# Kernel tuning notes

Hardware: AMD Instinct MI355X
Metric: run time of the kernel (lower is better)

Reference implementation:

```python
import jax, jax.numpy as jnp
import numpy as np

D = 4096
B_BITS = 4
NUM_CENTROIDS = 2 ** B_BITS  # 16 uniform centroids in [-1, 1]
N_TOKENS = 8192


def setup_inputs() -> dict:
    key = jax.random.key(0)
    kx, kp = jax.random.split(key)
    x = jax.random.normal(kx, (N_TOKENS, D), dtype=jnp.float32)
    # Orthogonal rotation Pi via QR of a random Gaussian (matches torch.linalg.qr)
    rand_mat = jax.random.normal(kp, (D, D), dtype=jnp.float32)
    Pi, _ = jnp.linalg.qr(rand_mat)
    centroids = jnp.linspace(-1.0, 1.0, NUM_CENTROIDS, dtype=jnp.float32)
    return {"x": x, "Pi": Pi, "centroids": centroids}


def _quantize(y, centroids):
    # Centroids are uniformly spaced on [-1, 1]; nearest-centroid argmin has the
    # closed form below (identical result to the broadcast |y - c| argmin, without
    # materializing the O(N*d*2^b) distance tensor).
    n = centroids.shape[0]
    scale = (n - 1) * 0.5
    idx = jnp.clip(jnp.round((y + 1.0) * scale), 0, n - 1).astype(jnp.int32)
    return centroids[idx]


def reference(x, Pi, centroids):
    y = x @ Pi.T                      # [N, d] rotate into quantization basis
    y_q = _quantize(y, centroids)     # nearest uniform centroid
    x_tilde = y_q @ Pi                # rotate back
    return x_tilde
```

## Files before the change

kernel.cpp:

```cpp
#include <hip/hip_runtime.h>
#include <hip/hip_bf16.h>

#define DD 4096
#define NTOK 8192

using u16 = unsigned short;

typedef __attribute__((ext_vector_type(8))) short bfrag;
typedef __attribute__((ext_vector_type(4))) float ffrag;
typedef __attribute__((ext_vector_type(4))) float f32x4v;

__device__ __forceinline__ u16 f2bf(float f) {
  unsigned u = __float_as_uint(f);
  u += 0x7FFFu + ((u >> 16) & 1u);
  return (u16)(u >> 16);
}
__device__ __forceinline__ float bf2f(u16 u) {
  return __uint_as_float(((unsigned)u) << 16);
}

#define GLDS16(g, l)                                                  \
  __builtin_amdgcn_global_load_lds(                                   \
      (__attribute__((address_space(1))) const void*)(g),             \
      (__attribute__((address_space(3))) void*)(l), 16, 0, 0)

#define MEMFENCE() asm volatile("" ::: "memory")

__global__ void __launch_bounds__(256) split_bf16_kernel(
    const float* __restrict__ in, u16* __restrict__ hi,
    u16* __restrict__ lo, long n4) {
  long i = (long)blockIdx.x * blockDim.x + threadIdx.x;
  const long stride = (long)gridDim.x * blockDim.x;
  for (; i < n4; i += stride) {
    f32x4v v = reinterpret_cast<const f32x4v*>(in)[i];
    u16 h[4], l[4];
#pragma unroll
    for (int j = 0; j < 4; ++j) {
      float f = v[j];
      u16 hb = f2bf(f);
      h[j] = hb;
      l[j] = f2bf(f - bf2f(hb));
    }
    ushort4 hv, lv;
    hv.x = h[0]; hv.y = h[1]; hv.z = h[2]; hv.w = h[3];
    lv.x = l[0]; lv.y = l[1]; lv.z = l[2]; lv.w = l[3];
    reinterpret_cast<ushort4*>(hi)[i] = hv;
    reinterpret_cast<ushort4*>(lo)[i] = lv;
  }
}

__global__ void __launch_bounds__(256) transpose_bf16_kernel(
    const float* __restrict__ in, u16* __restrict__ out, int R, int C) {
  __shared__ u16 tile[64][65];
  const int bc = blockIdx.x << 6;
  const int br = blockIdx.y << 6;
  const int tc = threadIdx.x & 63;
  const int tr0 = threadIdx.x >> 6;
#pragma unroll
  for (int p = 0; p < 16; ++p) {
    int r = tr0 + (p << 2);
    tile[tc][r] = f2bf(in[(size_t)(br + r) * C + (bc + tc)]);
  }
  __syncthreads();
#pragma unroll
  for (int p = 0; p < 16; ++p) {
    int orow = tr0 + (p << 2);
    out[(size_t)(bc + orow) * R + (br + tc)] = tile[orow][tc];
  }
}

__global__ void __launch_bounds__(512, 2) gemm_fused3_kernel(
    const u16* __restrict__ Ah_, const u16* __restrict__ Al_,
    const u16* __restrict__ Bh_, const u16* __restrict__ Bl_,
    u16* __restrict__ Yq, const float* __restrict__ cent, int M, int N) {
  __shared__ __align__(16) char SM[131072];
  __shared__ float clut[16];
  const int tid = threadIdx.x;
  if (tid < 16) clut[tid] = cent[tid];

  const int nbn = N >> 8;
  const int nwg = (M >> 8) * nbn;
  int wg = blockIdx.x;
  wg = (wg & 7) * (nwg >> 3) + (wg >> 3);
  const int tm = (wg / nbn) << 8;
  const int tn = (wg % nbn) << 8;

  const int lane = tid & 63;
  const int wv = tid >> 6;
  const int wm = wv >> 2;
  const int wn = wv & 3;
  const int l15 = lane & 15;
  const int kslc = lane >> 4;

  const int Dst = tid * 16;
  const int Lg = Dst ^ (((Dst >> 7) & 7) << 4);
  const int srow = Lg >> 6;
  const int scol = (Lg & 63) >> 1;
  const size_t sOffA = (size_t)(tm + srow) * 4096 + scol;
  const size_t sOffB = (size_t)(tn + srow) * 4096 + scol;

  auto STAGE = [&](int u, const u16* base, int tau) {
    if (tau >= 128) return;
    const u16* src = base + (u < 2 ? sOffA : sOffB) + tau * 32;
    char* lds = SM + (tau & 1) * 65536 + u * 16384 + Dst;
    GLDS16(src, lds);
    GLDS16(src + (size_t)128 * 4096, lds + 8192);
  };

  const int slot16 = ((((l15 & 1) << 2) | kslc) ^ (l15 >> 1)) << 4;
  const int aOff = wm * 8192 + (l15 >> 1) * 128 + slot16;
  const int bOff = wn * 4096 + (l15 >> 1) * 128 + slot16;

#define LDSF(b, ubase, off, f)                                           \
  (*reinterpret_cast<const bfrag*>(SM + (b) * 65536 + (ubase) + (off) +  \
                                   (f) * 1024))

  ffrag acc[8][4];
#pragma unroll
  for (int m = 0; m < 8; ++m)
#pragma unroll
    for (int n = 0; n < 4; ++n) acc[m][n] = {0.f, 0.f, 0.f, 0.f};

  bfrag Ahf[8], Alf[4], Bhf[4], Blf[4];

  STAGE(0, Ah_, 0); STAGE(1, Al_, 0); STAGE(2, Bh_, 0); STAGE(3, Bl_, 0);
  asm volatile("s_waitcnt vmcnt(2)" ::: "memory");
  MEMFENCE();
  __builtin_amdgcn_s_barrier();

#define MFMA16(Aset, a0, Bset, mb)                                       \
  __builtin_amdgcn_s_setprio(1);                                         \
  _Pragma("unroll")                                                      \
  for (int m = 0; m < 4; ++m)                                            \
    _Pragma("unroll")                                                    \
    for (int n = 0; n < 4; ++n)                                          \
      acc[(mb) + m][n] = __builtin_amdgcn_mfma_f32_16x16x32_bf16(        \
          Aset[(a0) + m], Bset[n], acc[(mb) + m][n], 0, 0, 0);           \
  __builtin_amdgcn_s_setprio(0);

  for (int t = 0; t < 128; ++t) {
    const int b = t & 1;
#pragma unroll
    for (int f = 0; f < 4; ++f) Ahf[f] = LDSF(b, 0, aOff, f);
#pragma unroll
    for (int f = 0; f < 4; ++f) Bhf[f] = LDSF(b, 32768, bOff, f);
    STAGE(0, Ah_, t + 1); STAGE(1, Al_, t + 1);
    MEMFENCE();
    __builtin_amdgcn_s_barrier();
    MFMA16(Ahf, 0, Bhf, 0)
    MEMFENCE();
    __builtin_amdgcn_s_barrier();
#pragma unroll
    for (int f = 0; f < 4; ++f) Ahf[4 + f] = LDSF(b, 0, aOff, 4 + f);
    STAGE(2, Bh_, t + 1); STAGE(3, Bl_, t + 1);
    MEMFENCE();
    __builtin_amdgcn_s_barrier();
    MFMA16(Ahf, 4, Bhf, 4)
    MEMFENCE();
    __builtin_amdgcn_s_barrier();
#pragma unroll
    for (int f = 0; f < 4; ++f) Alf[f] = LDSF(b, 16384, aOff, f);
    MEMFENCE();
    __builtin_amdgcn_s_barrier();
    MFMA16(Alf, 0, Bhf, 0)
    MEMFENCE();
    __builtin_amdgcn_s_barrier();
#pragma unroll
    for (int f = 0; f < 4; ++f) Alf[f] = LDSF(b, 16384, aOff, 4 + f);
    MEMFENCE();
    __builtin_amdgcn_s_barrier();
    MFMA16(Alf, 0, Bhf, 4)
    if (t < 127)
      asm volatile("s_waitcnt vmcnt(8)" ::: "memory");
    else
      asm volatile("s_waitcnt vmcnt(0)" ::: "memory");
    MEMFENCE();
    __builtin_amdgcn_s_barrier();
#pragma unroll
    for (int f = 0; f < 4; ++f) Blf[f] = LDSF(b, 49152, bOff, f);
    MEMFENCE();
    __builtin_amdgcn_s_barrier();
    MFMA16(Ahf, 0, Blf, 0)
    MFMA16(Ahf, 4, Blf, 4)
    asm volatile("s_waitcnt vmcnt(2)" ::: "memory");
    MEMFENCE();
    __builtin_amdgcn_s_barrier();
  }

  const int r0 = tm + wm * 128 + kslc * 4;
  const int c0 = tn + wn * 64 + l15;
#pragma unroll
  for (int m = 0; m < 8; ++m)
#pragma unroll
    for (int n = 0; n < 4; ++n)
#pragma unroll
      for (int r = 0; r < 4; ++r) {
        float y = acc[m][n][r];
        float s = rintf((y + 1.0f) * 7.5f);
        int idx = (int)s;
        idx = idx < 0 ? 0 : (idx > 15 ? 15 : idx);
        Yq[(size_t)(r0 + m * 16 + r) * N + (c0 + n * 16)] = f2bf(clut[idx]);
      }
#undef LDSF
#undef MFMA16
}

__global__ void __launch_bounds__(512, 2) gemm256_bt_kernel(
    const u16* __restrict__ A0, const u16* __restrict__ B0,
    float* __restrict__ Cout, int M, int N) {
  constexpr int NT = 64;
  __shared__ __align__(16) char SM[131072];
  const int tid = threadIdx.x;

  const int nbn = N >> 8;
  const int nwg = (M >> 8) * nbn;
  int wg = blockIdx.x;
  wg = (wg & 7) * (nwg >> 3) + (wg >> 3);
  const int tm = (wg / nbn) << 8;
  const int tn = (wg % nbn) << 8;

  const int lane = tid & 63;
  const int wv = tid >> 6;
  const int wm = wv >> 2;
  const int wn = wv & 3;
  const int l15 = lane & 15;
  const int kslc = lane >> 4;
  const int cXor = (lane & 7) << 4;

  const size_t thrOff =
      (size_t)(wv * 8 + (lane >> 3)) * 4096 + 8 * ((lane & 7) ^ (lane >> 3));
  const int ldsThr = wv * 1024 + lane * 16;

  auto STAGE = [&](int kind, int tau) {
    if (tau >= NT) return;
    const int b = tau & 1;
    const size_t ktE = (size_t)tau * 64;
    const u16* src;
    char* lds;
    if (kind >= 2) {
      const int idx = kind - 2;
      src = B0 + (size_t)(tn + idx * 128) * 4096 + ktE + thrOff;
      lds = SM + b * 65536 + 32768 + idx * 16384 + ldsThr;
    } else {
      src = A0 + (size_t)(tm + kind * 128) * 4096 + ktE + thrOff;
      lds = SM + b * 65536 + kind * 16384 + ldsThr;
    }
    GLDS16(src, lds);
    GLDS16(src + 262144, lds + 8192);
  };

#define LDSA(b, f, s)                                                      \
  (*reinterpret_cast<const bfrag*>(                                        \
      SM + (b) * 65536 + wm * 16384 + (((f) * 16 + l15) << 7) +            \
      ((((s) << 6) | (kslc << 4)) ^ cXor)))
#define LDSB(b, f, s)                                                      \
  (*reinterpret_cast<const bfrag*>(                                        \
      SM + (b) * 65536 + 32768 + (wn >> 1) * 16384 +                       \
      ((((wn & 1) * 64) + (f) * 16 + l15) << 7) +                          \
      ((((s) << 6) | (kslc << 4)) ^ cXor)))

  ffrag acc[8][4];
#pragma unroll
  for (int m = 0; m < 8; ++m)
#pragma unroll
    for (int n = 0; n < 4; ++n) acc[m][n] = {0.f, 0.f, 0.f, 0.f};

  STAGE(0, 0); STAGE(1, 0); STAGE(2, 0); STAGE(3, 0);
  STAGE(2, 1); STAGE(3, 1);
  asm volatile("s_waitcnt vmcnt(4)" ::: "memory");
  MEMFENCE();
  __builtin_amdgcn_s_barrier();

  bfrag Af[4], Bf[4];

  for (int t = 0; t < NT; ++t) {
    const int b = t & 1;
#pragma unroll
    for (int p = 0; p < 4; ++p) {
      const int s = p >> 1;
      const int mb = (p & 1) * 4;
      if ((p & 1) == 0) {
#pragma unroll
        for (int n = 0; n < 4; ++n) Bf[n] = LDSB(b, n, s);
      }
#pragma unroll
      for (int m = 0; m < 4; ++m) Af[m] = LDSA(b, mb + m, s);
      if (p == 0) STAGE(0, t + 1);
      else if (p == 1) STAGE(1, t + 1);
      else if (p == 3) { STAGE(2, t + 2); STAGE(3, t + 2); }
      MEMFENCE();
      __builtin_amdgcn_s_barrier();
      asm volatile("s_waitcnt lgkmcnt(0)" ::: "memory");
      __builtin_amdgcn_s_setprio(1);
#pragma unroll
      for (int m = 0; m < 4; ++m)
#pragma unroll
        for (int n = 0; n < 4; ++n)
          acc[mb + m][n] = __builtin_amdgcn_mfma_f32_16x16x32_bf16(
              Af[m], Bf[n], acc[mb + m][n], 0, 0, 0);
      __builtin_amdgcn_s_setprio(0);
      if (p == 3) {
        if (t == NT - 2)
          asm volatile("s_waitcnt vmcnt(0)" ::: "memory");
        else if (t < NT - 2)
          asm volatile("s_waitcnt vmcnt(4)" ::: "memory");
      }
      MEMFENCE();
      __builtin_amdgcn_s_barrier();
    }
  }

  const int r0 = tm + wm * 128 + kslc * 4;
  const int c0 = tn + wn * 64 + l15;
#pragma unroll
  for (int m = 0; m < 8; ++m)
#pragma unroll
    for (int n = 0; n < 4; ++n)
#pragma unroll
      for (int r = 0; r < 4; ++r)
        Cout[(size_t)(r0 + m * 16 + r) * N + (c0 + n * 16)] = acc[m][n][r];
#undef LDSA
#undef LDSB
}

extern "C" void kernel_launch(void* const* d_in, const int* in_sizes, int n_in,
                              void* d_out, int out_size, void* d_ws, size_t ws_size,
                              hipStream_t stream) {
  const float* x = (const float*)d_in[0];
  const float* Pi = (const float*)d_in[1];
  const float* cent = (const float*)d_in[2];
  float* out = (float*)d_out;

  const size_t MB = (size_t)1 << 20;
  if (ws_size < 288 * MB) return;

  char* ws = (char*)d_ws;
  u16* x_hi = (u16*)(ws + 0 * MB);
  u16* x_lo = (u16*)(ws + 64 * MB);
  u16* p_hi = (u16*)(ws + 128 * MB);
  u16* p_lo = (u16*)(ws + 160 * MB);
  u16* piT  = (u16*)(ws + 192 * MB);
  u16* yq   = (u16*)(ws + 224 * MB);

  split_bf16_kernel<<<2048, 256, 0, stream>>>(x, x_hi, x_lo, (long)NTOK * DD / 4);
  split_bf16_kernel<<<1024, 256, 0, stream>>>(Pi, p_hi, p_lo, (long)DD * DD / 4);
  transpose_bf16_kernel<<<dim3(DD / 64, DD / 64), 256, 0, stream>>>(Pi, piT, DD, DD);

  gemm_fused3_kernel<<<512, 512, 0, stream>>>(
      x_hi, x_lo, p_hi, p_lo, yq, cent, NTOK, DD);
  gemm256_bt_kernel<<<512, 512, 0, stream>>>(yq, piT, out, NTOK, DD);
}
```

Baseline: 1.014 ms.

## Replace bf16 low-part correction GEMMs with a single int8 MFMA correction term

The first GEMM used to compute three bf16 MFMA products (hi*hi, lo*hi, hi*lo) to emulate fp32 precision. It now computes hi*hi in bf16 and folds the two cross-correction terms into one int8 MFMA pass, using fixed-scale int8 quantizations of the x residual, x, Pi, and the Pi residual packed along K. Tiles shrink to 256x128 with a 1024-block grid and a reworked double-buffered staging schedule. The aim is to cut MFMA work and operand bandwidth for the correction terms. The cost is accuracy that depends on fixed quantization scales, which could misplace values near quantization boundaries.

```diff
diff --git a/kernel.cpp b/kernel.cpp
--- a/kernel.cpp
+++ b/kernel.cpp
@@ -7,6 +7,7 @@
 using u16 = unsigned short;
 
 typedef __attribute__((ext_vector_type(8))) short bfrag;
+typedef __attribute__((ext_vector_type(4))) int i32x4;
 typedef __attribute__((ext_vector_type(4))) float ffrag;
 typedef __attribute__((ext_vector_type(4))) float f32x4v;
 
@@ -18,6 +19,11 @@
 __device__ __forceinline__ float bf2f(u16 u) {
   return __uint_as_float(((unsigned)u) << 16);
 }
+__device__ __forceinline__ char q8(float v, float s) {
+  float r = rintf(v * s);
+  r = fminf(fmaxf(r, -127.f), 127.f);
+  return (char)(int)r;
+}
 
 #define GLDS16(g, l)                                                  \
   __builtin_amdgcn_global_load_lds(                                   \
@@ -26,26 +32,49 @@
 
 #define MEMFENCE() asm volatile("" ::: "memory")
 
-__global__ void __launch_bounds__(256) split_bf16_kernel(
+__global__ void __launch_bounds__(256) prep_x_kernel(
     const float* __restrict__ in, u16* __restrict__ hi,
-    u16* __restrict__ lo, long n4) {
+    char* __restrict__ lo8, char* __restrict__ hi8, long n4) {
   long i = (long)blockIdx.x * blockDim.x + threadIdx.x;
   const long stride = (long)gridDim.x * blockDim.x;
   for (; i < n4; i += stride) {
     f32x4v v = reinterpret_cast<const f32x4v*>(in)[i];
-    u16 h[4], l[4];
+    ushort4 hv; char4 lv, xv;
 #pragma unroll
     for (int j = 0; j < 4; ++j) {
       float f = v[j];
       u16 hb = f2bf(f);
-      h[j] = hb;
-      l[j] = f2bf(f - bf2f(hb));
-    }
-    ushort4 hv, lv;
-    hv.x = h[0]; hv.y = h[1]; hv.z = h[2]; hv.w = h[3];
-    lv.x = l[0]; lv.y = l[1]; lv.z = l[2]; lv.w = l[3];
+      float xl = f - bf2f(hb);
+      ((u16*)&hv)[j] = hb;
+      ((char*)&lv)[j] = q8(xl, 8192.f);
+      ((char*)&xv)[j] = q8(f, 16.f);
+    }
     reinterpret_cast<ushort4*>(hi)[i] = hv;
-    reinterpret_cast<ushort4*>(lo)[i] = lv;
+    reinterpret_cast<char4*>(lo8)[i] = lv;
+    reinterpret_cast<char4*>(hi8)[i] = xv;
+  }
+}
+
+__global__ void __launch_bounds__(256) prep_pi_kernel(
+    const float* __restrict__ in, u16* __restrict__ hi,
+    char* __restrict__ hi8, char* __restrict__ lo8, long n4) {
+  long i = (long)blockIdx.x * blockDim.x + threadIdx.x;
+  const long stride = (long)gridDim.x * blockDim.x;
+  for (; i < n4; i += stride) {
+    f32x4v v = reinterpret_cast<const f32x4v*>(in)[i];
+    ushort4 hv; char4 hq, lq;
+#pragma unroll
+    for (int j = 0; j < 4; ++j) {
+      float f = v[j];
+      u16 hb = f2bf(f);
+      float pl = f - bf2f(hb);
+      ((u16*)&hv)[j] = hb;
+      ((char*)&hq)[j] = q8(f, 1024.f);
+      ((char*)&lq)[j] = q8(pl, 524288.f);
+    }
+    reinterpret_cast<ushort4*>(hi)[i] = hv;
+    reinterpret_cast<char4*>(hi8)[i] = hq;
+    reinterpret_cast<char4*>(lo8)[i] = lq;
   }
 }
 
@@ -69,140 +98,150 @@
   }
 }
 
-__global__ void __launch_bounds__(512, 2) gemm_fused3_kernel(
-    const u16* __restrict__ Ah_, const u16* __restrict__ Al_,
-    const u16* __restrict__ Bh_, const u16* __restrict__ Bl_,
+__global__ void __launch_bounds__(512, 2) gemm_i8lo_kernel(
+    const u16* __restrict__ xh, const char* __restrict__ xl8,
+    const char* __restrict__ xh8, const u16* __restrict__ ph,
+    const char* __restrict__ ph8, const char* __restrict__ pl8,
     u16* __restrict__ Yq, const float* __restrict__ cent, int M, int N) {
-  __shared__ __align__(16) char SM[131072];
+  __shared__ __align__(16) char SM[98304];
   __shared__ float clut[16];
   const int tid = threadIdx.x;
   if (tid < 16) clut[tid] = cent[tid];
 
-  const int nbn = N >> 8;
+  const int nbn = N >> 7;
   const int nwg = (M >> 8) * nbn;
   int wg = blockIdx.x;
   wg = (wg & 7) * (nwg >> 3) + (wg >> 3);
   const int tm = (wg / nbn) << 8;
-  const int tn = (wg % nbn) << 8;
+  const int tn = (wg % nbn) << 7;
 
   const int lane = tid & 63;
   const int wv = tid >> 6;
-  const int wm = wv >> 2;
-  const int wn = wv & 3;
+  const int wm = wv >> 1;
+  const int wn = wv & 1;
   const int l15 = lane & 15;
   const int kslc = lane >> 4;
 
-  const int Dst = tid * 16;
-  const int Lg = Dst ^ (((Dst >> 7) & 7) << 4);
-  const int srow = Lg >> 6;
-  const int scol = (Lg & 63) >> 1;
-  const size_t sOffA = (size_t)(tm + srow) * 4096 + scol;
-  const size_t sOffB = (size_t)(tn + srow) * 4096 + scol;
-
-  auto STAGE = [&](int u, const u16* base, int tau) {
+  const int D0 = tid * 16, D1 = D0 + 8192;
+  const int L0 = D0 ^ (((D0 >> 7) & 3) << 4);
+  const int L1 = D1 ^ (((D1 >> 7) & 3) << 4);
+  const int row0 = D0 >> 6, row1 = D1 >> 6;
+  const int colE0 = (L0 & 63) >> 1, colE1 = (L1 & 63) >> 1;
+  const int sel0 = (L0 & 63) >> 5, col80 = L0 & 31;
+  const int sel1 = (L1 & 63) >> 5, col81 = L1 & 31;
+
+  const u16* pAh0 = xh + (size_t)(tm + row0) * 4096 + colE0;
+  const u16* pAh1 = xh + (size_t)(tm + row1) * 4096 + colE1;
+  const char* pA80 = (sel0 ? xh8 : xl8) + (size_t)(tm + row0) * 4096 + col80;
+  const char* pA81 = (sel1 ? xh8 : xl8) + (size_t)(tm + row1) * 4096 + col81;
+  const u16* pBh = ph + (size_t)(tn + row0) * 4096 + colE0;
+  const char* pB8 = (sel0 ? pl8 : ph8) + (size_t)(tn + row0) * 4096 + col80;
+
+  auto stageA = [&](int tau) {
     if (tau >= 128) return;
-    const u16* src = base + (u < 2 ? sOffA : sOffB) + tau * 32;
-    char* lds = SM + (tau & 1) * 65536 + u * 16384 + Dst;
-    GLDS16(src, lds);
-    GLDS16(src + (size_t)128 * 4096, lds + 8192);
+    char* base = SM + (tau & 1) * 49152;
+    const int o = tau * 32;
+    GLDS16(pAh0 + o, base + D0);
+    GLDS16(pAh1 + o, base + D0 + 8192);
+    GLDS16(pA80 + o, base + 16384 + D0);
+    GLDS16(pA81 + o, base + 16384 + D0 + 8192);
   };
-
-  const int slot16 = ((((l15 & 1) << 2) | kslc) ^ (l15 >> 1)) << 4;
-  const int aOff = wm * 8192 + (l15 >> 1) * 128 + slot16;
-  const int bOff = wn * 4096 + (l15 >> 1) * 128 + slot16;
-
-#define LDSF(b, ubase, off, f)                                           \
-  (*reinterpret_cast<const bfrag*>(SM + (b) * 65536 + (ubase) + (off) +  \
-                                   (f) * 1024))
-
-  ffrag acc[8][4];
-#pragma unroll
-  for (int m = 0; m < 8; ++m)
-#pragma unroll
-    for (int n = 0; n < 4; ++n) acc[m][n] = {0.f, 0.f, 0.f, 0.f};
-
-  bfrag Ahf[8], Alf[4], Bhf[4], Blf[4];
-
-  STAGE(0, Ah_, 0); STAGE(1, Al_, 0); STAGE(2, Bh_, 0); STAGE(3, Bl_, 0);
+  auto stageB = [&](int tau) {
+    if (tau >= 128) return;
+    char* base = SM + (tau & 1) * 49152;
+    const int o = tau * 32;
+    GLDS16(pBh + o, base + 32768 + D0);
+    GLDS16(pB8 + o, base + 40960 + D0);
+  };
+
+  int aoff[4], boff[4];
+#pragma unroll
+  for (int i = 0; i < 4; ++i) {
+    const int rA = wm * 64 + i * 16 + l15;
+    aoff[i] = rA * 64 + ((kslc ^ ((rA >> 1) & 3)) << 4);
+    const int rB = wn * 64 + i * 16 + l15;
+    boff[i] = rB * 64 + ((kslc ^ ((rB >> 1) & 3)) << 4);
+  }
+
+  ffrag acc[4][4];
+  i32x4 accq[4][4];
+#pragma unroll
+  for (int m = 0; m < 4; ++m)
+#pragma unroll
+    for (int n = 0; n < 4; ++n) {
+      acc[m][n] = {0.f, 0.f, 0.f, 0.f};
+      accq[m][n] = {0, 0, 0, 0};
+    }
+
+  stageA(0); stageB(0); stageB(1);
   asm volatile("s_waitcnt vmcnt(2)" ::: "memory");
   MEMFENCE();
   __builtin_amdgcn_s_barrier();
 
-#define MFMA16(Aset, a0, Bset, mb)                                       \
-  __builtin_amdgcn_s_setprio(1);                                         \
-  _Pragma("unroll")                                                      \
-  for (int m = 0; m < 4; ++m)                                            \
-    _Pragma("unroll")                                                    \
-    for (int n = 0; n < 4; ++n)                                          \
-      acc[(mb) + m][n] = __builtin_amdgcn_mfma_f32_16x16x32_bf16(        \
-          Aset[(a0) + m], Bset[n], acc[(mb) + m][n], 0, 0, 0);           \
-  __builtin_amdgcn_s_setprio(0);
+  bfrag Ahf[4], Bhf[4];
+  i32x4 A8f[4], B8f[4];
 
   for (int t = 0; t < 128; ++t) {
-    const int b = t & 1;
-#pragma unroll
-    for (int f = 0; f < 4; ++f) Ahf[f] = LDSF(b, 0, aOff, f);
-#pragma unroll
-    for (int f = 0; f < 4; ++f) Bhf[f] = LDSF(b, 32768, bOff, f);
-    STAGE(0, Ah_, t + 1); STAGE(1, Al_, t + 1);
+    const char* base = SM + (t & 1) * 49152;
+#pragma unroll
+    for (int i = 0; i < 4; ++i)
+      Ahf[i] = *reinterpret_cast<const bfrag*>(base + aoff[i]);
+#pragma unroll
+    for (int i = 0; i < 4; ++i)
+      Bhf[i] = *reinterpret_cast<const bfrag*>(base + 32768 + boff[i]);
+#pragma unroll
+    for (int i = 0; i < 4; ++i)
+      A8f[i] = *reinterpret_cast<const i32x4*>(base + 16384 + aoff[i]);
+#pragma unroll
+    for (int i = 0; i < 4; ++i)
+      B8f[i] = *reinterpret_cast<const i32x4*>(base + 40960 + boff[i]);
+    stageA(t + 1);
     MEMFENCE();
     __builtin_amdgcn_s_barrier();
-    MFMA16(Ahf, 0, Bhf, 0)
+    __builtin_amdgcn_s_setprio(1);
+#pragma unroll
+    for (int m = 0; m < 4; ++m)
+#pragma unroll
+      for (int n = 0; n < 4; ++n)
+        acc[m][n] = __builtin_amdgcn_mfma_f32_16x16x32_bf16(
+            Ahf[m], Bhf[n], acc[m][n], 0, 0, 0);
+    __builtin_amdgcn_s_setprio(0);
+    asm volatile("s_waitcnt lgkmcnt(0)" ::: "memory");
     MEMFENCE();
     __builtin_amdgcn_s_barrier();
-#pragma unroll
-    for (int f = 0; f < 4; ++f) Ahf[4 + f] = LDSF(b, 0, aOff, 4 + f);
-    STAGE(2, Bh_, t + 1); STAGE(3, Bl_, t + 1);
+    stageB(t + 2);
     MEMFENCE();
     __builtin_amdgcn_s_barrier();
-    MFMA16(Ahf, 4, Bhf, 4)
+    __builtin_amdgcn_s_setprio(1);
+#pragma unroll
+    for (int m = 0; m < 4; ++m)
+#pragma unroll
+      for (int n = 0; n < 4; ++n)
+        accq[m][n] = __builtin_amdgcn_mfma_i32_16x16x64_i8(
+            A8f[m], B8f[n], accq[m][n], 0, 0, 0);
+    __builtin_amdgcn_s_setprio(0);
+    if (t >= 126)
+      asm volatile("s_waitcnt vmcnt(0)" ::: "memory");
+    else
+      asm volatile("s_waitcnt vmcnt(2)" ::: "memory");
     MEMFENCE();
     __builtin_amdgcn_s_barrier();
-#pragma unroll
-    for (int f = 0; f < 4; ++f) Alf[f] = LDSF(b, 16384, aOff, f);
-    MEMFENCE();
-    __builtin_amdgcn_s_barrier();
-    MFMA16(Alf, 0, Bhf, 0)
-    MEMFENCE();
-    __builtin_amdgcn_s_barrier();
-#pragma unroll
-    for (int f = 0; f < 4; ++f) Alf[f] = LDSF(b, 16384, aOff, 4 + f);
-    MEMFENCE();
-    __builtin_amdgcn_s_barrier();
-    MFMA16(Alf, 0, Bhf, 4)
-    if (t < 127)
-      asm volatile("s_waitcnt vmcnt(8)" ::: "memory");
-    else
-      asm volatile("s_waitcnt vmcnt(0)" ::: "memory");
-    MEMFENCE();
-    __builtin_amdgcn_s_barrier();
-#pragma unroll
-    for (int f = 0; f < 4; ++f) Blf[f] = LDSF(b, 49152, bOff, f);
-    MEMFENCE();
-    __builtin_amdgcn_s_barrier();
-    MFMA16(Ahf, 0, Blf, 0)
-    MFMA16(Ahf, 4, Blf, 4)
-    asm volatile("s_waitcnt vmcnt(2)" ::: "memory");
-    MEMFENCE();
-    __builtin_amdgcn_s_barrier();
-  }
-
-  const int r0 = tm + wm * 128 + kslc * 4;
+  }
+
+  const int r0 = tm + wm * 64 + kslc * 4;
   const int c0 = tn + wn * 64 + l15;
 #pragma unroll
-  for (int m = 0; m < 8; ++m)
+  for (int m = 0; m < 4; ++m)
 #pragma unroll
     for (int n = 0; n < 4; ++n)
 #pragma unroll
       for (int r = 0; r < 4; ++r) {
-        float y = acc[m][n][r];
+        float y = acc[m][n][r] + (float)accq[m][n][r] * 0x1p-23f;
         float s = rintf((y + 1.0f) * 7.5f);
         int idx = (int)s;
         idx = idx < 0 ? 0 : (idx > 15 ? 15 : idx);
         Yq[(size_t)(r0 + m * 16 + r) * N + (c0 + n * 16)] = f2bf(clut[idx]);
       }
-#undef LDSF
-#undef MFMA16
 }
 
 __global__ void __launch_bounds__(512, 2) gemm256_bt_kernel(
@@ -335,18 +374,22 @@
   if (ws_size < 288 * MB) return;
 
   char* ws = (char*)d_ws;
-  u16* x_hi = (u16*)(ws + 0 * MB);
-  u16* x_lo = (u16*)(ws + 64 * MB);
-  u16* p_hi = (u16*)(ws + 128 * MB);
-  u16* p_lo = (u16*)(ws + 160 * MB);
-  u16* piT  = (u16*)(ws + 192 * MB);
-  u16* yq   = (u16*)(ws + 224 * MB);
-
-  split_bf16_kernel<<<2048, 256, 0, stream>>>(x, x_hi, x_lo, (long)NTOK * DD / 4);
-  split_bf16_kernel<<<1024, 256, 0, stream>>>(Pi, p_hi, p_lo, (long)DD * DD / 4);
+  u16* x_hi  = (u16*)(ws + 0 * MB);
+  char* x_lo8 = (char*)(ws + 64 * MB);
+  char* x_hi8 = (char*)(ws + 96 * MB);
+  u16* p_hi  = (u16*)(ws + 128 * MB);
+  char* p_hi8 = (char*)(ws + 160 * MB);
+  char* p_lo8 = (char*)(ws + 176 * MB);
+  u16* piT   = (u16*)(ws + 192 * MB);
+  u16* yq    = (u16*)(ws + 224 * MB);
+
+  prep_x_kernel<<<2048, 256, 0, stream>>>(x, x_hi, x_lo8, x_hi8,
+                                          (long)NTOK * DD / 4);
+  prep_pi_kernel<<<2048, 256, 0, stream>>>(Pi, p_hi, p_hi8, p_lo8,
+                                           (long)DD * DD / 4);
   transpose_bf16_kernel<<<dim3(DD / 64, DD / 64), 256, 0, stream>>>(Pi, piT, DD, DD);
 
-  gemm_fused3_kernel<<<512, 512, 0, stream>>>(
-      x_hi, x_lo, p_hi, p_lo, yq, cent, NTOK, DD);
+  gemm_i8lo_kernel<<<1024, 512, 0, stream>>>(
+      x_hi, x_lo8, x_hi8, p_hi, p_hi8, p_lo8, yq, cent, NTOK, DD);
   gemm256_bt_kernel<<<512, 512, 0, stream>>>(yq, piT, out, NTOK, DD);
 }
```

Result: slower. 1.150 ms (+13.4%).

## Shrink fused split-bf16 GEMM tile to 256x128 with single-buffered in-place staging

Applied to the files above, without the earlier changes.

The first GEMM (3-term split-bf16 rotation plus quantize) now uses 256-thread workgroups on 256x128 output tiles, launched as 1024 blocks. The LDS double buffer is dropped in favour of a single 48KB buffer. Each operand's next K-slice is staged into its own region once that region's fragments have been read into registers, guarded by lgkmcnt waits and barriers. The goal is to cut LDS use so more workgroups fit per CU and to overlap global loads with MFMA inside one buffer, at the cost of less overlap slack and more B-matrix reloads.

```diff
diff --git a/kernel.cpp b/kernel.cpp
--- a/kernel.cpp
+++ b/kernel.cpp
@@ -69,51 +69,59 @@
   }
 }
 
-__global__ void __launch_bounds__(512, 2) gemm_fused3_kernel(
+__global__ void __launch_bounds__(256, 2) gemm_fused3_kernel(
     const u16* __restrict__ Ah_, const u16* __restrict__ Al_,
     const u16* __restrict__ Bh_, const u16* __restrict__ Bl_,
     u16* __restrict__ Yq, const float* __restrict__ cent, int M, int N) {
-  __shared__ __align__(16) char SM[131072];
+  __shared__ __align__(16) char SM[49152];
   __shared__ float clut[16];
   const int tid = threadIdx.x;
   if (tid < 16) clut[tid] = cent[tid];
 
-  const int nbn = N >> 8;
+  const int nbn = N >> 7;
   const int nwg = (M >> 8) * nbn;
   int wg = blockIdx.x;
   wg = (wg & 7) * (nwg >> 3) + (wg >> 3);
   const int tm = (wg / nbn) << 8;
-  const int tn = (wg % nbn) << 8;
+  const int tn = (wg % nbn) << 7;
 
   const int lane = tid & 63;
   const int wv = tid >> 6;
-  const int wm = wv >> 2;
-  const int wn = wv & 3;
+  const int wm = wv >> 1;
+  const int wn = wv & 1;
   const int l15 = lane & 15;
   const int kslc = lane >> 4;
 
-  const int Dst = tid * 16;
-  const int Lg = Dst ^ (((Dst >> 7) & 7) << 4);
-  const int srow = Lg >> 6;
-  const int scol = (Lg & 63) >> 1;
-  const size_t sOffA = (size_t)(tm + srow) * 4096 + scol;
-  const size_t sOffB = (size_t)(tn + srow) * 4096 + scol;
-
-  auto STAGE = [&](int u, const u16* base, int tau) {
+  const int key = (tid >> 3) & 7;
+  const int baseL = (tid * 16) ^ (key << 4);
+  const int srow = baseL >> 6;
+  const int scol = (baseL & 63) >> 1;
+  const size_t sA = (size_t)(tm + srow) * 4096 + scol;
+  const size_t sB = (size_t)(tn + srow) * 4096 + scol;
+  const int dOff = tid * 16;
+
+  auto STAGE_A = [&](const u16* g, int ubase, int tau) {
     if (tau >= 128) return;
-    const u16* src = base + (u < 2 ? sOffA : sOffB) + tau * 32;
-    char* lds = SM + (tau & 1) * 65536 + u * 16384 + Dst;
+    const u16* src = g + sA + (size_t)tau * 32;
+    char* lds = SM + ubase + dOff;
+#pragma unroll
+    for (int q = 0; q < 4; ++q)
+      GLDS16(src + (size_t)q * 64 * 4096, lds + q * 4096);
+  };
+  auto STAGE_B = [&](const u16* g, int ubase, int tau) {
+    if (tau >= 128) return;
+    const u16* src = g + sB + (size_t)tau * 32;
+    char* lds = SM + ubase + dOff;
     GLDS16(src, lds);
-    GLDS16(src + (size_t)128 * 4096, lds + 8192);
+    GLDS16(src + (size_t)64 * 4096, lds + 4096);
   };
 
   const int slot16 = ((((l15 & 1) << 2) | kslc) ^ (l15 >> 1)) << 4;
   const int aOff = wm * 8192 + (l15 >> 1) * 128 + slot16;
   const int bOff = wn * 4096 + (l15 >> 1) * 128 + slot16;
 
-#define LDSF(b, ubase, off, f)                                           \
-  (*reinterpret_cast<const bfrag*>(SM + (b) * 65536 + (ubase) + (off) +  \
-                                   (f) * 1024))
+#define LDSF(ubase, off, f)                                              \
+  (*reinterpret_cast<const bfrag*>(SM + (ubase) + (off) + (f) * 1024))
 
   ffrag acc[8][4];
 #pragma unroll
@@ -123,7 +131,8 @@
 
   bfrag Ahf[8], Alf[4], Bhf[4], Blf[4];
 
-  STAGE(0, Ah_, 0); STAGE(1, Al_, 0); STAGE(2, Bh_, 0); STAGE(3, Bl_, 0);
+  STAGE_A(Ah_, 0, 0); STAGE_A(Al_, 16384, 0);
+  STAGE_B(Bh_, 32768, 0); STAGE_B(Bl_, 40960, 0);
   asm volatile("s_waitcnt vmcnt(2)" ::: "memory");
   MEMFENCE();
   __builtin_amdgcn_s_barrier();
@@ -139,47 +148,51 @@
   __builtin_amdgcn_s_setprio(0);
 
   for (int t = 0; t < 128; ++t) {
-    const int b = t & 1;
-#pragma unroll
-    for (int f = 0; f < 4; ++f) Ahf[f] = LDSF(b, 0, aOff, f);
-#pragma unroll
-    for (int f = 0; f < 4; ++f) Bhf[f] = LDSF(b, 32768, bOff, f);
-    STAGE(0, Ah_, t + 1); STAGE(1, Al_, t + 1);
+#pragma unroll
+    for (int f = 0; f < 4; ++f) Ahf[f] = LDSF(0, aOff, f);
+#pragma unroll
+    for (int f = 0; f < 4; ++f) Bhf[f] = LDSF(32768, bOff, f);
     MEMFENCE();
     __builtin_amdgcn_s_barrier();
     MFMA16(Ahf, 0, Bhf, 0)
     MEMFENCE();
     __builtin_amdgcn_s_barrier();
 #pragma unroll
-    for (int f = 0; f < 4; ++f) Ahf[4 + f] = LDSF(b, 0, aOff, 4 + f);
-    STAGE(2, Bh_, t + 1); STAGE(3, Bl_, t + 1);
-    MEMFENCE();
-    __builtin_amdgcn_s_barrier();
+    for (int f = 0; f < 4; ++f) Ahf[4 + f] = LDSF(0, aOff, 4 + f);
+    asm volatile("s_waitcnt lgkmcnt(0)" ::: "memory");
+    MEMFENCE();
+    __builtin_amdgcn_s_barrier();
+    STAGE_A(Ah_, 0, t + 1);
     MFMA16(Ahf, 4, Bhf, 4)
     MEMFENCE();
     __builtin_amdgcn_s_barrier();
 #pragma unroll
-    for (int f = 0; f < 4; ++f) Alf[f] = LDSF(b, 16384, aOff, f);
+    for (int f = 0; f < 4; ++f) Alf[f] = LDSF(16384, aOff, f);
     MEMFENCE();
     __builtin_amdgcn_s_barrier();
     MFMA16(Alf, 0, Bhf, 0)
     MEMFENCE();
     __builtin_amdgcn_s_barrier();
 #pragma unroll
-    for (int f = 0; f < 4; ++f) Alf[f] = LDSF(b, 16384, aOff, 4 + f);
-    MEMFENCE();
-    __builtin_amdgcn_s_barrier();
+    for (int f = 0; f < 4; ++f) Alf[f] = LDSF(16384, aOff, 4 + f);
+    asm volatile("s_waitcnt lgkmcnt(0)" ::: "memory");
+    MEMFENCE();
+    __builtin_amdgcn_s_barrier();
+    STAGE_A(Al_, 16384, t + 1);
+    STAGE_B(Bh_, 32768, t + 1);
     MFMA16(Alf, 0, Bhf, 4)
     if (t < 127)
-      asm volatile("s_waitcnt vmcnt(8)" ::: "memory");
+      asm volatile("s_waitcnt vmcnt(10)" ::: "memory");
     else
       asm volatile("s_waitcnt vmcnt(0)" ::: "memory");
     MEMFENCE();
     __builtin_amdgcn_s_barrier();
 #pragma unroll
-    for (int f = 0; f < 4; ++f) Blf[f] = LDSF(b, 49152, bOff, f);
-    MEMFENCE();
-    __builtin_amdgcn_s_barrier();
+    for (int f = 0; f < 4; ++f) Blf[f] = LDSF(40960, bOff, f);
+    asm volatile("s_waitcnt lgkmcnt(0)" ::: "memory");
+    MEMFENCE();
+    __builtin_amdgcn_s_barrier();
+    STAGE_B(Bl_, 40960, t + 1);
     MFMA16(Ahf, 0, Blf, 0)
     MFMA16(Ahf, 4, Blf, 4)
     asm volatile("s_waitcnt vmcnt(2)" ::: "memory");
@@ -346,7 +359,7 @@
   split_bf16_kernel<<<1024, 256, 0, stream>>>(Pi, p_hi, p_lo, (long)DD * DD / 4);
   transpose_bf16_kernel<<<dim3(DD / 64, DD / 64), 256, 0, stream>>>(Pi, piT, DD, DD);
 
-  gemm_fused3_kernel<<<512, 512, 0, stream>>>(
+  gemm_fused3_kernel<<<1024, 256, 0, stream>>>(
       x_hi, x_lo, p_hi, p_lo, yq, cent, NTOK, DD);
   gemm256_bt_kernel<<<512, 512, 0, stream>>>(yq, piT, out, NTOK, DD);
 }
```

New measurement: 996.5 us. Within noise of the previous version (-1.7%).
